# Kernel tuning notes

Hardware: AMD Instinct MI355X
Metric: run time of the kernel (lower is better)

Reference implementation:

```python
import jax, jax.numpy as jnp
import numpy as np

HEAD_NUM = 16
MASK_FILL = 100000.0  # source uses +1e5 on masked entries (not -inf)


def setup_inputs() -> dict:
    key = jax.random.key(0)
    k1, k2, k3, k4, k5 = jax.random.split(key, 5)
    B, S, E = 2, 2048, 1024
    scale = 0.02
    return {
        "x": jax.random.normal(k1, (B, S, E), dtype=jnp.float32),
        "W_atten": jax.random.normal(k2, (E, 3 * E), dtype=jnp.float32) * scale,
        "b_atten": jax.random.normal(k3, (3 * E,), dtype=jnp.float32) * scale,
        "W_proj": jax.random.normal(k4, (E, E), dtype=jnp.float32) * scale,
        "b_proj": jax.random.normal(k5, (E,), dtype=jnp.float32) * scale,
    }


def reference(x, W_atten, b_atten, W_proj, b_proj):
    B, S, E = x.shape
    H = HEAD_NUM
    hd = E // H
    # QKV projection: [B, S, 3E]
    qkv = x @ W_atten + b_atten
    # reshape [B, S, H, 3*hd] -> [B, H, S, 3*hd], chunk into q,k,v [B,H,S,hd]
    qkv = jnp.transpose(qkv.reshape(B, S, H, 3 * hd), (0, 2, 1, 3))
    q, k, v = jnp.split(qkv, 3, axis=-1)
    # raw scores, NO 1/sqrt(dk) scaling (faithful to source)
    w = jnp.einsum("bhqd,bhkd->bhqk", q, k)
    # causal mask applied as w*mask + (1-mask)*1e5 (faithful to source)
    mask = jnp.tril(jnp.ones((S, S), dtype=w.dtype))
    w = w * mask + (1.0 - mask) * MASK_FILL
    # softmax over dim=1 == HEAD axis (faithful to source quirk)
    w = jax.nn.softmax(w, axis=1)
    # attn_drop: identity in eval mode
    a = jnp.einsum("bhqk,bhkd->bhqd", w, v)  # [B,H,S,hd]
    a = jnp.transpose(a, (0, 2, 1, 3)).reshape(B, S, E)
    h = a @ W_proj + b_proj
    # resi_drop: identity in eval mode
    return h
```

## Files before the change

### kernel.cpp

```cpp
#include <hip/hip_runtime.h>

#define DI __device__ __forceinline__

typedef __attribute__((ext_vector_type(8))) short s16x8;
typedef __attribute__((ext_vector_type(4))) short s16x4;
typedef __attribute__((ext_vector_type(4))) float f32x4;

DI unsigned short f2bf(float f){
  unsigned u = __float_as_uint(f);
  u = (u + 0x7FFFu + ((u >> 16) & 1u)) >> 16;
  return (unsigned short)u;
}
DI float bf2f(unsigned short h){
  return __uint_as_float(((unsigned)h) << 16);
}
DI float exp2i(float x){ float r; asm("v_exp_f32 %0, %1" : "=v"(r) : "v"(x)); return r; }

DI void gll16(const void* g, void* l){
  __builtin_amdgcn_global_load_lds((const __attribute__((address_space(1))) void*)g,
                                   (__attribute__((address_space(3))) void*)l, 16, 0, 0);
}

#define VMCNT(n) asm volatile("s_waitcnt vmcnt(" #n ")" ::: "memory")

__global__ void cvt_kernel(const float* __restrict__ in, unsigned short* __restrict__ out, int n8){
  int i = blockIdx.x * blockDim.x + threadIdx.x;
  if (i >= n8) return;
  const float4* p = (const float4*)in + (size_t)i * 2;
  float4 a = p[0], b = p[1];
  s16x8 o;
  o[0] = (short)f2bf(a.x); o[1] = (short)f2bf(a.y); o[2] = (short)f2bf(a.z); o[3] = (short)f2bf(a.w);
  o[4] = (short)f2bf(b.x); o[5] = (short)f2bf(b.y); o[6] = (short)f2bf(b.z); o[7] = (short)f2bf(b.w);
  ((s16x8*)out)[i] = o;
}

__global__ void transpose_cvt(const float* __restrict__ in, unsigned short* __restrict__ out, int R, int C){
  __shared__ float t[32][33];
  int c0 = blockIdx.x * 32, r0 = blockIdx.y * 32;
  int tx = threadIdx.x, ty = threadIdx.y;
  #pragma unroll
  for (int i = 0; i < 4; i++)
    t[ty + i*8][tx] = in[(size_t)(r0 + ty + i*8) * C + c0 + tx];
  __syncthreads();
  #pragma unroll
  for (int i = 0; i < 4; i++)
    out[(size_t)(c0 + ty + i*8) * R + r0 + tx] = f2bf(t[tx][ty + i*8]);
}

template<int MODE, int BM>
__launch_bounds__(256)
__global__ void gemm_kernel(const unsigned short* __restrict__ A,
                            const unsigned short* __restrict__ Wt,
                            const float* __restrict__ bias,
                            int N,
                            unsigned short* __restrict__ qb,
                            unsigned short* __restrict__ kb,
                            unsigned short* __restrict__ vt,
                            float* __restrict__ out)
{
  constexpr int MI = BM / 32;
  constexpr int AC = BM / 32;
  const int K = 1024;
  __shared__ unsigned short As[BM * 64];
  __shared__ unsigned short Bs[128 * 64];
  int m0 = blockIdx.y * BM, n0 = blockIdx.x * 128;
  int tid = threadIdx.x;
  int lane = tid & 63, w = tid >> 6;
  int row_l = lane & 15, kgrp = lane >> 4;
  int wm = (w >> 1) * (MI * 16), wn = (w & 1) * 64;

  const unsigned short* asrc[AC];
  const unsigned short* bsrc[4];
  int ldsoA[AC], ldsoB[4];
  int chunk = (lane & 7) ^ (lane >> 3);
  #pragma unroll
  for (int c4 = 0; c4 < AC; c4++){
    int r = c4*32 + w*8 + (lane >> 3);
    asrc[c4] = A + (size_t)(m0 + r) * K + chunk*8;
    ldsoA[c4] = (c4*32 + w*8) * 64;
  }
  #pragma unroll
  for (int c4 = 0; c4 < 4; c4++){
    int r = c4*32 + w*8 + (lane >> 3);
    bsrc[c4] = Wt + (size_t)(n0 + r) * K + chunk*8;
    ldsoB[c4] = (c4*32 + w*8) * 64;
  }
  int eA[MI], eB[4];
  #pragma unroll
  for (int i = 0; i < MI; i++){
    int ra = wm + i*16 + row_l;
    eA[i] = (ra*64 + kgrp*8) ^ ((ra & 7) << 3);
  }
  #pragma unroll
  for (int i = 0; i < 4; i++){
    int rb = wn + i*16 + row_l;
    eB[i] = (rb*64 + kgrp*8) ^ ((rb & 7) << 3);
  }

  f32x4 acc[MI][4];
  #pragma unroll
  for (int i = 0; i < MI; i++)
    #pragma unroll
    for (int j = 0; j < 4; j++)
      acc[i][j] = (f32x4){0.f, 0.f, 0.f, 0.f};

  for (int k0 = 0; k0 < K; k0 += 64){
    #pragma unroll
    for (int c4 = 0; c4 < AC; c4++)
      gll16(asrc[c4] + k0, (void*)(As + ldsoA[c4]));
    #pragma unroll
    for (int c4 = 0; c4 < 4; c4++)
      gll16(bsrc[c4] + k0, (void*)(Bs + ldsoB[c4]));
    __syncthreads();
    #pragma unroll
    for (int kc = 0; kc < 2; kc++){
      s16x8 af[MI], bfr[4];
      #pragma unroll
      for (int mi = 0; mi < MI; mi++)
        af[mi] = *(const s16x8*)&As[eA[mi] ^ (kc*32)];
      #pragma unroll
      for (int ni = 0; ni < 4; ni++)
        bfr[ni] = *(const s16x8*)&Bs[eB[ni] ^ (kc*32)];
      #pragma unroll
      for (int mi = 0; mi < MI; mi++)
        #pragma unroll
        for (int ni = 0; ni < 4; ni++)
          acc[mi][ni] = __builtin_amdgcn_mfma_f32_16x16x32_bf16(af[mi], bfr[ni], acc[mi][ni], 0, 0, 0);
    }
    __syncthreads();
  }

  #pragma unroll
  for (int mi = 0; mi < MI; mi++){
    #pragma unroll
    for (int ni = 0; ni < 4; ni++){
      #pragma unroll
      for (int j = 0; j < 4; j++){
        int gr = m0 + wm + mi*16 + kgrp*4 + j;
        int gc = n0 + wn + ni*16 + row_l;
        float v = acc[mi][ni][j] + bias[gc];
        if (MODE == 0){
          int h = gc / 192, cc = gc % 192;
          int b = gr >> 11, s = gr & 2047;
          if (cc < 64){
            qb[(size_t)gr * 1024 + h*64 + cc] = f2bf(v * 1.44269504f);
          } else if (cc < 128){
            int d = cc - 64; int kt = s >> 6, kk = s & 63;
            kb[(size_t)((b*16 + h)*32 + kt) * 4096 + ((kk*64 + d) ^ ((kk & 7) << 3))] = f2bf(v);
          } else {
            int d = cc - 128; int kt = s >> 6, kk = s & 63;
            vt[(size_t)((b*16 + h)*32 + kt) * 4096 + ((d*64 + kk) ^ ((d & 7) << 3))] = f2bf(v);
          }
        } else {
          out[(size_t)gr * N + gc] = v;
        }
      }
    }
  }
}

__global__ void sufv_kernel(const unsigned short* __restrict__ vt, float* __restrict__ sufv){
  __shared__ float tot[4][64];
  int bh = blockIdx.x;
  int tid = threadIdx.x;
  int tq = tid >> 6, d = tid & 63;
  const unsigned short* base = vt + (size_t)bh * 32 * 4096;
  float s[8];
  float run = 0.f;
  for (int j = 7; j >= 0; j--){
    int t = tq*8 + j;
    float rs = 0.f;
    #pragma unroll
    for (int c = 0; c < 8; c++){
      int idx = (d*64 + c*8) ^ ((d & 7) << 3);
      s16x8 v = *(const s16x8*)&base[(size_t)t*4096 + idx];
      #pragma unroll
      for (int e = 0; e < 8; e++) rs += bf2f((unsigned short)v[e]);
    }
    run += rs; s[j] = run;
  }
  tot[tq][d] = run;
  __syncthreads();
  float carry = 0.f;
  for (int t2 = tq+1; t2 < 4; t2++) carry += tot[t2][d];
  #pragma unroll
  for (int j = 0; j < 8; j++)
    sufv[((size_t)bh*33 + tq*8 + j)*64 + d] = s[j] + carry;
  if (tid < 64) sufv[((size_t)bh*33 + 32)*64 + tid] = 0.f;
}

__launch_bounds__(256)
__global__ void dpass_kernel(const unsigned short* __restrict__ qbuf,
                             const unsigned short* __restrict__ kb,
                             unsigned short* __restrict__ invb)
{
  __shared__ unsigned short Kst[4][4096];
  int bid = blockIdx.x;
  int blk = (bid & 7) * 132 + (bid >> 3);
  int b = blk / 528, t = blk % 528;
  int kt = (int)(32.5f - sqrtf(1056.25f - 2.f*t));
  while (kt*(65-kt)/2 > t) kt--;
  while ((kt+1)*(64-kt)/2 <= t) kt++;
  int qt = kt + (t - kt*(65-kt)/2);

  int tid = threadIdx.x, lane = tid & 63, w = tid >> 6;
  int row_l = lane & 15, kgrp = lane >> 4;

  const unsigned short* ktb = kb + ((size_t)(b*16)*32 + kt) * 4096;
  int sgoff = (w*128 + lane)*8;

  auto stage = [&](int hh, int buf){
    const unsigned short* src = ktb + (size_t)hh * 131072;
    gll16(src + sgoff,       (void*)(&Kst[buf][0] + w*1024));
    gll16(src + sgoff + 512, (void*)(&Kst[buf][0] + w*1024 + 512));
  };

  int e0[4];
  #pragma unroll
  for (int ks = 0; ks < 4; ks++){
    int row = ks*16 + row_l;
    e0[ks] = (row*64 + kgrp*8) ^ ((row & 7) << 3);
  }

  stage(0, 0);
  stage(1, 1);

  f32x4 esum[4];
  #pragma unroll
  for (int ks = 0; ks < 4; ks++) esum[ks] = (f32x4){0.f,0.f,0.f,0.f};

  const unsigned short* qrow_p = qbuf + (size_t)(b*2048 + qt*64 + w*16 + row_l) * 1024;
  s16x8 qf0 = *(const s16x8*)&qrow_p[kgrp*8];
  s16x8 qf1 = *(const s16x8*)&qrow_p[32 + kgrp*8];

  for (int h = 0; h < 16; h++){
    s16x8 qn0, qn1;
    if (h < 15){
      qn0 = *(const s16x8*)&qrow_p[(h+1)*64 + kgrp*8];
      qn1 = *(const s16x8*)&qrow_p[(h+1)*64 + 32 + kgrp*8];
    }
    if (h + 2 < 16) stage(h+2, (h+2) & 3);
    __builtin_amdgcn_sched_barrier(0);
    if (h < 14)      VMCNT(8);
    else if (h < 15) VMCNT(6);
    else             VMCNT(2);
    __builtin_amdgcn_sched_barrier(0);
    __builtin_amdgcn_s_barrier();
    __builtin_amdgcn_sched_barrier(0);

    const unsigned short* kl = &Kst[h & 3][0];
    #pragma unroll
    for (int ks = 0; ks < 4; ks++){
      s16x8 a0 = *(const s16x8*)&kl[e0[ks]];
      s16x8 a1 = *(const s16x8*)&kl[e0[ks] ^ 32];
      f32x4 sc = __builtin_amdgcn_mfma_f32_16x16x32_bf16(a0, qf0, (f32x4){0.f,0.f,0.f,0.f}, 0, 0, 0);
      sc = __builtin_amdgcn_mfma_f32_16x16x32_bf16(a1, qf1, sc, 0, 0, 0);
      #pragma unroll
      for (int j = 0; j < 4; j++) esum[ks][j] += exp2i(sc[j]);
    }
    if (h < 15){ qf0 = qn0; qf1 = qn1; }
  }

  int qcol = qt*64 + w*16 + row_l;
  unsigned short* dst = invb + (size_t)b*4194304 + (size_t)qcol*2048 + kt*64 + kgrp*4;
  #pragma unroll
  for (int ks = 0; ks < 4; ks++){
    float r0 = 1.f/esum[ks][0], r1 = 1.f/esum[ks][1];
    float r2 = 1.f/esum[ks][2], r3 = 1.f/esum[ks][3];
    unsigned lo, hi;
    asm("v_cvt_pk_bf16_f32 %0, %1, %2" : "=v"(lo) : "v"(r0), "v"(r1));
    asm("v_cvt_pk_bf16_f32 %0, %1, %2" : "=v"(hi) : "v"(r2), "v"(r3));
    uint2 pk; pk.x = lo; pk.y = hi;
    *(uint2*)&dst[ks*16] = pk;
  }
}

__launch_bounds__(256)
__global__ void pv_kernel(const unsigned short* __restrict__ qbuf,
                          const unsigned short* __restrict__ kb,
                          const unsigned short* __restrict__ vt,
                          const unsigned short* __restrict__ invb,
                          const float* __restrict__ sufv,
                          unsigned short* __restrict__ ab,
                          float* __restrict__ pb)
{
  __shared__ unsigned short Kst[4][4096];
  __shared__ unsigned short Vst[2][4096];
  __shared__ unsigned short Wsh[4][1152];

  int blk = ((blockIdx.x & 7) << 7) + (blockIdx.x >> 3);
  int b = blk >> 9;
  int r = blk & 511;
  int h = r >> 5;
  int r2 = r & 31;
  int i = r2 >> 1, half = r2 & 1;
  int qsm = i, qbig = 31 - i;

  int tid = threadIdx.x, lane = tid & 63, w = tid >> 6;
  int row_l = lane & 15, kgrp = lane >> 4;

  const unsigned short* KT = kb + (size_t)((b*16 + h)*32) * 4096;
  const unsigned short* VT = vt + (size_t)((b*16 + h)*32) * 4096;
  int sgoff = (w*128 + lane)*8;
  unsigned short* Wsw = &Wsh[w][0];

  int eK[4];
  #pragma unroll
  for (int ks = 0; ks < 4; ks++){
    int row = ks*16 + row_l;
    eK[ks] = (row*64 + kgrp*8) ^ ((row & 7) << 3);
  }

  auto stageK = [&](int kt, int buf){
    gll16(KT + (size_t)kt*4096 + sgoff,       (void*)(&Kst[buf][0] + w*1024));
    gll16(KT + (size_t)kt*4096 + sgoff + 512, (void*)(&Kst[buf][0] + w*1024 + 512));
  };
  auto stageV = [&](int kt, int buf){
    gll16(VT + (size_t)kt*4096 + sgoff,       (void*)(&Vst[buf][0] + w*1024));
    gll16(VT + (size_t)kt*4096 + sgoff + 512, (void*)(&Vst[buf][0] + w*1024 + 512));
  };

  auto run = [&](int qt, int k0t, int k1t, int mode){
    int q0 = qt * 64;
    int qv = q0 + w*16 + row_l;
    const unsigned short* qrow_p = qbuf + (size_t)(b*2048 + qv) * 1024 + h*64;
    s16x8 qf0 = *(const s16x8*)&qrow_p[kgrp*8];
    s16x8 qf1 = *(const s16x8*)&qrow_p[32 + kgrp*8];
    const unsigned short* ivrow = invb + (size_t)b*4194304 + (size_t)qv*2048 + kgrp*4;

    f32x4 pvv[4];
    #pragma unroll
    for (int d = 0; d < 4; d++) pvv[d] = (f32x4){0.f,0.f,0.f,0.f};

    __syncthreads();
    stageK(k0t, k0t & 3);
    stageV(k0t, k0t & 1);
    s16x4 i1[4];
    #pragma unroll
    for (int ks = 0; ks < 4; ks++) i1[ks] = *(const s16x4*)&ivrow[k0t*64 + ks*16];
    if (k0t + 1 < k1t) stageK(k0t+1, (k0t+1) & 3);

    for (int kt = k0t; kt < k1t; kt++){
      bool nx1 = (kt + 1 < k1t), nx2 = (kt + 2 < k1t);
      bool first = (kt == k0t);

      s16x4 icur[4];
      #pragma unroll
      for (int ks = 0; ks < 4; ks++) icur[ks] = i1[ks];
      if (nx1){
        #pragma unroll
        for (int ks = 0; ks < 4; ks++) i1[ks] = *(const s16x4*)&ivrow[(kt+1)*64 + ks*16];
      }
      if (nx2) stageK(kt+2, (kt+2) & 3);

      __builtin_amdgcn_sched_barrier(0);
      if (first){
        if (nx2)      VMCNT(12);
        else if (nx1) VMCNT(10);
        else          VMCNT(4);
      } else {
        if (nx2)      VMCNT(6);
        else if (nx1) VMCNT(4);
        else          VMCNT(0);
      }
      __builtin_amdgcn_sched_barrier(0);
      __builtin_amdgcn_s_barrier();
      __builtin_amdgcn_sched_barrier(0);

      if (nx1) stageV(kt+1, (kt+1) & 1);

      const unsigned short* kl = &Kst[kt & 3][0];
      const unsigned short* vl = &Vst[kt & 1][0];
      f32x4 sc[4];
      #pragma unroll
      for (int ks = 0; ks < 4; ks++){
        s16x8 a0 = *(const s16x8*)&kl[eK[ks]];
        s16x8 a1 = *(const s16x8*)&kl[eK[ks] ^ 32];
        sc[ks] = __builtin_amdgcn_mfma_f32_16x16x32_bf16(a0, qf0, (f32x4){0.f,0.f,0.f,0.f}, 0, 0, 0);
        sc[ks] = __builtin_amdgcn_mfma_f32_16x16x32_bf16(a1, qf1, sc[ks], 0, 0, 0);
      }

      if (kt == qt){
        int kbase = kt*64 + kgrp*4;
        #pragma unroll
        for (int ks = 0; ks < 4; ks++){
          #pragma unroll
          for (int j = 0; j < 4; j++){
            float wv = exp2i(sc[ks][j]) * bf2f((unsigned short)icur[ks][j]);
            sc[ks][j] = (kbase + ks*16 + j > qv) ? 0.0625f : wv;
          }
          unsigned lo, hi;
          asm("v_cvt_pk_bf16_f32 %0, %1, %2" : "=v"(lo) : "v"(sc[ks][0]), "v"(sc[ks][1]));
          asm("v_cvt_pk_bf16_f32 %0, %1, %2" : "=v"(hi) : "v"(sc[ks][2]), "v"(sc[ks][3]));
          uint2 pk2; pk2.x = lo; pk2.y = hi;
          *(uint2*)&Wsw[row_l*72 + ks*16 + kgrp*4] = pk2;
        }
      } else {
        #pragma unroll
        for (int ks = 0; ks < 4; ks++){
          #pragma unroll
          for (int j = 0; j < 4; j++)
            sc[ks][j] = exp2i(sc[ks][j]) * bf2f((unsigned short)icur[ks][j]);
          unsigned lo, hi;
          asm("v_cvt_pk_bf16_f32 %0, %1, %2" : "=v"(lo) : "v"(sc[ks][0]), "v"(sc[ks][1]));
          asm("v_cvt_pk_bf16_f32 %0, %1, %2" : "=v"(hi) : "v"(sc[ks][2]), "v"(sc[ks][3]));
          uint2 pk2; pk2.x = lo; pk2.y = hi;
          *(uint2*)&Wsw[row_l*72 + ks*16 + kgrp*4] = pk2;
        }
      }

      #pragma unroll
      for (int kc = 0; kc < 2; kc++){
        s16x8 af = *(const s16x8*)&Wsw[row_l*72 + kc*32 + kgrp*8];
        #pragma unroll
        for (int dq = 0; dq < 4; dq++){
          s16x8 vf = *(const s16x8*)&vl[eK[dq] ^ (kc*32)];
          pvv[dq] = __builtin_amdgcn_mfma_f32_16x16x32_bf16(af, vf, pvv[dq], 0, 0, 0);
        }
      }
    }

    if (mode == 0){
      int tsuf = qt + 1;
      #pragma unroll
      for (int dq = 0; dq < 4; dq++){
        int d = dq*16 + row_l;
        float suf = sufv[((size_t)(b*16 + h)*33 + tsuf)*64 + d];
        #pragma unroll
        for (int j = 0; j < 4; j++){
          int qo = q0 + w*16 + kgrp*4 + j;
          ab[(size_t)(b*2048 + qo)*1024 + h*64 + d] = f2bf(pvv[dq][j] + 0.0625f * suf);
        }
      }
    } else {
      float* pr = pb + ((size_t)((b*16 + h)*16 + i)*2 + (mode - 1)) * 4096;
      #pragma unroll
      for (int dq = 0; dq < 4; dq++){
        int d = dq*16 + row_l;
        #pragma unroll
        for (int j = 0; j < 4; j++)
          pr[(w*16 + kgrp*4 + j)*64 + d] = pvv[dq][j];
      }
    }
  };

  if (half == 0){
    run(qsm, 0, i + 1, 0);
    run(qbig, 0, 16 - i, 1);
  } else {
    run(qbig, 16 - i, 32 - i, 2);
  }
}

__global__ void reduce_kernel(const float* __restrict__ pb,
                              const float* __restrict__ sufv,
                              unsigned short* __restrict__ ab)
{
  int blk = blockIdx.x;
  int b = blk >> 8, rr = blk & 255;
  int h = rr >> 4, i = rr & 15;
  int qbig = 31 - i, tsuf = 32 - i;
  int t = threadIdx.x;
  int q = t >> 2, dbase = (t & 3) * 16;
  const float* p0 = pb + ((size_t)((b*16 + h)*16 + i)*2 + 0)*4096 + q*64 + dbase;
  const float* p1 = p0 + 4096;
  const float* sf = sufv + ((size_t)(b*16 + h)*33 + tsuf)*64 + dbase;
  unsigned short* op = ab + (size_t)(b*2048 + qbig*64 + q)*1024 + h*64 + dbase;
  #pragma unroll
  for (int e = 0; e < 4; e++){
    float4 a = *(const float4*)(p0 + e*4);
    float4 bb = *(const float4*)(p1 + e*4);
    float4 s = *(const float4*)(sf + e*4);
    unsigned short o[4];
    o[0] = f2bf(a.x + bb.x + 0.0625f * s.x);
    o[1] = f2bf(a.y + bb.y + 0.0625f * s.y);
    o[2] = f2bf(a.z + bb.z + 0.0625f * s.z);
    o[3] = f2bf(a.w + bb.w + 0.0625f * s.w);
    *(s16x4*)(op + e*4) = *(s16x4*)o;
  }
}

extern "C" void kernel_launch(void* const* d_in, const int* in_sizes, int n_in,
                              void* d_out, int out_size, void* d_ws, size_t ws_size,
                              hipStream_t stream) {
  (void)in_sizes; (void)n_in; (void)out_size; (void)ws_size;
  const float* x  = (const float*)d_in[0];
  const float* Wa = (const float*)d_in[1];
  const float* ba = (const float*)d_in[2];
  const float* Wp = (const float*)d_in[3];
  const float* bp = (const float*)d_in[4];
  float* out = (float*)d_out;

  char* ws = (char*)d_ws;
  size_t off = 0;
  auto alloc = [&](size_t bytes) -> void* {
    void* p = ws + off;
    off += (bytes + 255) & ~(size_t)255;
    return p;
  };
  float* pbuf          = (float*)alloc((size_t)16*1024*1024);
  unsigned short* xb   = (unsigned short*)((char*)pbuf);
  unsigned short* WaT  = (unsigned short*)((char*)pbuf + (size_t)4096*1024*2);
  unsigned short* WpT  = (unsigned short*)alloc((size_t)1024*1024*2);
  unsigned short* qbuf = (unsigned short*)alloc((size_t)4096*1024*2);
  unsigned short* ktile= (unsigned short*)alloc((size_t)4096*1024*2);
  unsigned short* vtile= (unsigned short*)alloc((size_t)4096*1024*2);
  unsigned short* abuf = (unsigned short*)alloc((size_t)4096*1024*2);
  unsigned short* invb = (unsigned short*)alloc((size_t)2*2048*2048*2);
  float* sufv          = (float*)alloc((size_t)32*33*64*4);

  cvt_kernel<<<2048, 256, 0, stream>>>(x, xb, 4096*1024/8);
  transpose_cvt<<<dim3(3072/32, 1024/32), dim3(32, 8), 0, stream>>>(Wa, WaT, 1024, 3072);
  transpose_cvt<<<dim3(1024/32, 1024/32), dim3(32, 8), 0, stream>>>(Wp, WpT, 1024, 1024);

  gemm_kernel<0,128><<<dim3(24, 32), 256, 0, stream>>>(xb, WaT, ba, 3072, qbuf, ktile, vtile, nullptr);

  sufv_kernel<<<32, 256, 0, stream>>>(vtile, sufv);

  dpass_kernel<<<1056, 256, 0, stream>>>(qbuf, ktile, invb);

  pv_kernel<<<1024, 256, 0, stream>>>(qbuf, ktile, vtile, invb, sufv, abuf, pbuf);

  reduce_kernel<<<512, 256, 0, stream>>>(pbuf, sufv, abuf);

  gemm_kernel<1,64><<<dim3(1024/128, 4096/64), 256, 0, stream>>>(abuf, WpT, bp, 1024, nullptr, nullptr, nullptr, out);
}
```

Measured before the change: 180.6 us.

## Drop split-K partials in PV kernel and stage V-tile epilogue through LDS

The PV kernel no longer splits the large query tile's key range across two blocks with fp32 partials and a separate reduce kernel. Each block now processes one paired small/large query tile over its full key range and writes the bf16 result directly, which removes the partial-buffer traffic and one launch. The cost is half as many blocks (512) and less even load balance per block. The QKV GEMM epilogue also packs V outputs into LDS, transposes them there, and writes them as 16-byte vector stores instead of scattered 2-byte stores.

Measured after the change: 164.6 us. 8.8% less time.

```diff
diff --git a/kernel.cpp b/kernel.cpp
--- a/kernel.cpp
+++ b/kernel.cpp
@@ -22,6 +22,7 @@
 }
 
 #define VMCNT(n) asm volatile("s_waitcnt vmcnt(" #n ")" ::: "memory")
+#define SB() __builtin_amdgcn_sched_barrier(0)
 
 __global__ void cvt_kernel(const float* __restrict__ in, unsigned short* __restrict__ out, int n8){
   int i = blockIdx.x * blockDim.x + threadIdx.x;
@@ -61,8 +62,9 @@
   constexpr int MI = BM / 32;
   constexpr int AC = BM / 32;
   const int K = 1024;
-  __shared__ unsigned short As[BM * 64];
-  __shared__ unsigned short Bs[128 * 64];
+  __shared__ __align__(16) unsigned short Sm[BM*64 + 128*64];
+  unsigned short* As = Sm;
+  unsigned short* Bs = Sm + BM*64;
   int m0 = blockIdx.y * BM, n0 = blockIdx.x * 128;
   int tid = threadIdx.x;
   int lane = tid & 63, w = tid >> 6;
@@ -130,29 +132,65 @@
     __syncthreads();
   }
 
-  #pragma unroll
-  for (int mi = 0; mi < MI; mi++){
-    #pragma unroll
-    for (int ni = 0; ni < 4; ni++){
-      #pragma unroll
-      for (int j = 0; j < 4; j++){
-        int gr = m0 + wm + mi*16 + kgrp*4 + j;
-        int gc = n0 + wn + ni*16 + row_l;
-        float v = acc[mi][ni][j] + bias[gc];
-        if (MODE == 0){
-          int h = gc / 192, cc = gc % 192;
-          int b = gr >> 11, s = gr & 2047;
-          if (cc < 64){
-            qb[(size_t)gr * 1024 + h*64 + cc] = f2bf(v * 1.44269504f);
-          } else if (cc < 128){
-            int d = cc - 64; int kt = s >> 6, kk = s & 63;
-            kb[(size_t)((b*16 + h)*32 + kt) * 4096 + ((kk*64 + d) ^ ((kk & 7) << 3))] = f2bf(v);
-          } else {
-            int d = cc - 128; int kt = s >> 6, kk = s & 63;
-            vt[(size_t)((b*16 + h)*32 + kt) * 4096 + ((d*64 + kk) ^ ((d & 7) << 3))] = f2bf(v);
+  if (MODE == 0){
+    unsigned long long* ldsT = (unsigned long long*)Sm;
+    #pragma unroll
+    for (int mi = 0; mi < MI; mi++){
+      #pragma unroll
+      for (int ni = 0; ni < 4; ni++){
+        int np = wn + ni*16 + row_l;
+        int gc = n0 + np;
+        int hh = gc / 192, cc = gc % 192;
+        float bia = bias[gc];
+        if (cc < 128){
+          #pragma unroll
+          for (int j = 0; j < 4; j++){
+            int gr = m0 + wm + mi*16 + kgrp*4 + j;
+            float v = acc[mi][ni][j] + bia;
+            if (cc < 64){
+              qb[(size_t)gr * 1024 + hh*64 + cc] = f2bf(v * 1.44269504f);
+            } else {
+              int d = cc - 64; int b = gr >> 11, s = gr & 2047;
+              int kt = s >> 6, kk = s & 63;
+              kb[(size_t)((b*16 + hh)*32 + kt) * 4096 + ((kk*64 + d) ^ ((kk & 7) << 3))] = f2bf(v);
+            }
           }
         } else {
-          out[(size_t)gr * N + gc] = v;
+          float v0 = acc[mi][ni][0] + bia, v1 = acc[mi][ni][1] + bia;
+          float v2 = acc[mi][ni][2] + bia, v3 = acc[mi][ni][3] + bia;
+          unsigned lo, hi;
+          asm("v_cvt_pk_bf16_f32 %0, %1, %2" : "=v"(lo) : "v"(v0), "v"(v1));
+          asm("v_cvt_pk_bf16_f32 %0, %1, %2" : "=v"(hi) : "v"(v2), "v"(v3));
+          int mq = (wm + mi*16 + kgrp*4) >> 2;
+          ldsT[np*32 + (mq ^ ((np & 7) << 2))] = ((unsigned long long)hi << 32) | (unsigned long long)lo;
+        }
+      }
+    }
+    __syncthreads();
+    int bb = m0 >> 11, s_base = m0 & 2047;
+    for (int item = tid; item < 2048; item += 256){
+      int np = item >> 4;
+      int gcv = n0 + np;
+      int cc = gcv % 192;
+      if (cc < 128) continue;
+      int d = cc - 128, hh = gcv / 192;
+      int sub = (item >> 3) & 1;
+      int c = item & 7;
+      int mq0 = sub*16 + c*2;
+      s16x8 val = *(const s16x8*)&Sm[np*128 + ((mq0 ^ ((np & 7) << 2)) << 2)];
+      size_t base = ((size_t)((bb*16 + hh)*32) + (s_base >> 6) + sub) * 4096 + d*64 + ((c ^ (d & 7)) << 3);
+      *(s16x8*)&vt[base] = val;
+    }
+  } else {
+    #pragma unroll
+    for (int mi = 0; mi < MI; mi++){
+      #pragma unroll
+      for (int ni = 0; ni < 4; ni++){
+        #pragma unroll
+        for (int j = 0; j < 4; j++){
+          int gr = m0 + wm + mi*16 + kgrp*4 + j;
+          int gc = n0 + wn + ni*16 + row_l;
+          out[(size_t)gr * N + gc] = acc[mi][ni][j] + bias[gc];
         }
       }
     }
@@ -240,13 +278,13 @@
       qn1 = *(const s16x8*)&qrow_p[(h+1)*64 + 32 + kgrp*8];
     }
     if (h + 2 < 16) stage(h+2, (h+2) & 3);
-    __builtin_amdgcn_sched_barrier(0);
+    SB();
     if (h < 14)      VMCNT(8);
     else if (h < 15) VMCNT(6);
     else             VMCNT(2);
-    __builtin_amdgcn_sched_barrier(0);
+    SB();
     __builtin_amdgcn_s_barrier();
-    __builtin_amdgcn_sched_barrier(0);
+    SB();
 
     const unsigned short* kl = &Kst[h & 3][0];
     #pragma unroll
@@ -281,20 +319,17 @@
                           const unsigned short* __restrict__ vt,
                           const unsigned short* __restrict__ invb,
                           const float* __restrict__ sufv,
-                          unsigned short* __restrict__ ab,
-                          float* __restrict__ pb)
+                          unsigned short* __restrict__ ab)
 {
   __shared__ unsigned short Kst[4][4096];
   __shared__ unsigned short Vst[2][4096];
   __shared__ unsigned short Wsh[4][1152];
 
-  int blk = ((blockIdx.x & 7) << 7) + (blockIdx.x >> 3);
-  int b = blk >> 9;
-  int r = blk & 511;
-  int h = r >> 5;
-  int r2 = r & 31;
-  int i = r2 >> 1, half = r2 & 1;
-  int qsm = i, qbig = 31 - i;
+  int bid = blockIdx.x;
+  int blk = ((bid & 7) << 6) | (bid >> 3);
+  int i = blk & 15;
+  int h = (blk >> 4) & 15;
+  int b = blk >> 8;
 
   int tid = threadIdx.x, lane = tid & 63, w = tid >> 6;
   int row_l = lane & 15, kgrp = lane >> 4;
@@ -320,12 +355,13 @@
     gll16(VT + (size_t)kt*4096 + sgoff + 512, (void*)(&Vst[buf][0] + w*1024 + 512));
   };
 
-  auto run = [&](int qt, int k0t, int k1t, int mode){
+  auto run = [&](int qt, int k1t){
     int q0 = qt * 64;
     int qv = q0 + w*16 + row_l;
     const unsigned short* qrow_p = qbuf + (size_t)(b*2048 + qv) * 1024 + h*64;
     s16x8 qf0 = *(const s16x8*)&qrow_p[kgrp*8];
     s16x8 qf1 = *(const s16x8*)&qrow_p[32 + kgrp*8];
+    SB();
     const unsigned short* ivrow = invb + (size_t)b*4194304 + (size_t)qv*2048 + kgrp*4;
 
     f32x4 pvv[4];
@@ -333,16 +369,17 @@
     for (int d = 0; d < 4; d++) pvv[d] = (f32x4){0.f,0.f,0.f,0.f};
 
     __syncthreads();
-    stageK(k0t, k0t & 3);
-    stageV(k0t, k0t & 1);
+    stageK(0, 0);
+    stageV(0, 0);
     s16x4 i1[4];
     #pragma unroll
-    for (int ks = 0; ks < 4; ks++) i1[ks] = *(const s16x4*)&ivrow[k0t*64 + ks*16];
-    if (k0t + 1 < k1t) stageK(k0t+1, (k0t+1) & 3);
-
-    for (int kt = k0t; kt < k1t; kt++){
+    for (int ks = 0; ks < 4; ks++) i1[ks] = *(const s16x4*)&ivrow[ks*16];
+    if (1 < k1t) stageK(1, 1);
+    SB();
+
+    for (int kt = 0; kt < k1t; kt++){
       bool nx1 = (kt + 1 < k1t), nx2 = (kt + 2 < k1t);
-      bool first = (kt == k0t);
+      bool first = (kt == 0);
 
       s16x4 icur[4];
       #pragma unroll
@@ -351,9 +388,9 @@
         #pragma unroll
         for (int ks = 0; ks < 4; ks++) i1[ks] = *(const s16x4*)&ivrow[(kt+1)*64 + ks*16];
       }
+      SB();
       if (nx2) stageK(kt+2, (kt+2) & 3);
-
-      __builtin_amdgcn_sched_barrier(0);
+      SB();
       if (first){
         if (nx2)      VMCNT(12);
         else if (nx1) VMCNT(10);
@@ -363,11 +400,11 @@
         else if (nx1) VMCNT(4);
         else          VMCNT(0);
       }
-      __builtin_amdgcn_sched_barrier(0);
+      SB();
       __builtin_amdgcn_s_barrier();
-      __builtin_amdgcn_sched_barrier(0);
-
+      SB();
       if (nx1) stageV(kt+1, (kt+1) & 1);
+      SB();
 
       const unsigned short* kl = &Kst[kt & 3][0];
       const unsigned short* vl = &Vst[kt & 1][0];
@@ -420,64 +457,21 @@
       }
     }
 
-    if (mode == 0){
-      int tsuf = qt + 1;
-      #pragma unroll
-      for (int dq = 0; dq < 4; dq++){
-        int d = dq*16 + row_l;
-        float suf = sufv[((size_t)(b*16 + h)*33 + tsuf)*64 + d];
-        #pragma unroll
-        for (int j = 0; j < 4; j++){
-          int qo = q0 + w*16 + kgrp*4 + j;
-          ab[(size_t)(b*2048 + qo)*1024 + h*64 + d] = f2bf(pvv[dq][j] + 0.0625f * suf);
-        }
-      }
-    } else {
-      float* pr = pb + ((size_t)((b*16 + h)*16 + i)*2 + (mode - 1)) * 4096;
-      #pragma unroll
-      for (int dq = 0; dq < 4; dq++){
-        int d = dq*16 + row_l;
-        #pragma unroll
-        for (int j = 0; j < 4; j++)
-          pr[(w*16 + kgrp*4 + j)*64 + d] = pvv[dq][j];
+    int tsuf = qt + 1;
+    #pragma unroll
+    for (int dq = 0; dq < 4; dq++){
+      int d = dq*16 + row_l;
+      float suf = sufv[((size_t)(b*16 + h)*33 + tsuf)*64 + d];
+      #pragma unroll
+      for (int j = 0; j < 4; j++){
+        int qo = q0 + w*16 + kgrp*4 + j;
+        ab[(size_t)(b*2048 + qo)*1024 + h*64 + d] = f2bf(pvv[dq][j] + 0.0625f * suf);
       }
     }
   };
 
-  if (half == 0){
-    run(qsm, 0, i + 1, 0);
-    run(qbig, 0, 16 - i, 1);
-  } else {
-    run(qbig, 16 - i, 32 - i, 2);
-  }
-}
-
-__global__ void reduce_kernel(const float* __restrict__ pb,
-                              const float* __restrict__ sufv,
-                              unsigned short* __restrict__ ab)
-{
-  int blk = blockIdx.x;
-  int b = blk >> 8, rr = blk & 255;
-  int h = rr >> 4, i = rr & 15;
-  int qbig = 31 - i, tsuf = 32 - i;
-  int t = threadIdx.x;
-  int q = t >> 2, dbase = (t & 3) * 16;
-  const float* p0 = pb + ((size_t)((b*16 + h)*16 + i)*2 + 0)*4096 + q*64 + dbase;
-  const float* p1 = p0 + 4096;
-  const float* sf = sufv + ((size_t)(b*16 + h)*33 + tsuf)*64 + dbase;
-  unsigned short* op = ab + (size_t)(b*2048 + qbig*64 + q)*1024 + h*64 + dbase;
-  #pragma unroll
-  for (int e = 0; e < 4; e++){
-    float4 a = *(const float4*)(p0 + e*4);
-    float4 bb = *(const float4*)(p1 + e*4);
-    float4 s = *(const float4*)(sf + e*4);
-    unsigned short o[4];
-    o[0] = f2bf(a.x + bb.x + 0.0625f * s.x);
-    o[1] = f2bf(a.y + bb.y + 0.0625f * s.y);
-    o[2] = f2bf(a.z + bb.z + 0.0625f * s.z);
-    o[3] = f2bf(a.w + bb.w + 0.0625f * s.w);
-    *(s16x4*)(op + e*4) = *(s16x4*)o;
-  }
+  run(i, i + 1);
+  run(31 - i, 32 - i);
 }
 
 extern "C" void kernel_launch(void* const* d_in, const int* in_sizes, int n_in,
@@ -498,9 +492,8 @@
     off += (bytes + 255) & ~(size_t)255;
     return p;
   };
-  float* pbuf          = (float*)alloc((size_t)16*1024*1024);
-  unsigned short* xb   = (unsigned short*)((char*)pbuf);
-  unsigned short* WaT  = (unsigned short*)((char*)pbuf + (size_t)4096*1024*2);
+  unsigned short* xb   = (unsigned short*)alloc((size_t)4096*1024*2);
+  unsigned short* WaT  = (unsigned short*)alloc((size_t)3072*1024*2);
   unsigned short* WpT  = (unsigned short*)alloc((size_t)1024*1024*2);
   unsigned short* qbuf = (unsigned short*)alloc((size_t)4096*1024*2);
   unsigned short* ktile= (unsigned short*)alloc((size_t)4096*1024*2);
@@ -519,9 +512,7 @@
 
   dpass_kernel<<<1056, 256, 0, stream>>>(qbuf, ktile, invb);
 
-  pv_kernel<<<1024, 256, 0, stream>>>(qbuf, ktile, vtile, invb, sufv, abuf, pbuf);
-
-  reduce_kernel<<<512, 256, 0, stream>>>(pbuf, sufv, abuf);
+  pv_kernel<<<512, 256, 0, stream>>>(qbuf, ktile, vtile, invb, sufv, abuf);
 
   gemm_kernel<1,64><<<dim3(1024/128, 4096/64), 256, 0, stream>>>(abuf, WpT, bp, 1024, nullptr, nullptr, nullptr, out);
 }
```
